# Performance work log

Measured on AMD Instinct MI355X. Metric: run time of the kernel, lower is better.

## Reference

```python
import jax, jax.numpy as jnp
import numpy as np

B, NQ, NK, D = 8, 2048, 2048, 1024

def setup_inputs() -> dict:
    key = jax.random.key(0)
    k1, k2, k3, k4, k5 = jax.random.split(key, 5)
    query_input = jax.random.normal(k1, (B, NQ, D), dtype=jnp.float32)
    key_input = jax.random.normal(k2, (B, NK, D), dtype=jnp.float32)
    s = 1.0 / np.sqrt(D)
    # nn.Linear(in,out,bias=False): y = x @ W.T, W shape (out,in)
    Wq = jax.random.uniform(k3, (D, D), dtype=jnp.float32, minval=-s, maxval=s)
    Wk = jax.random.uniform(k4, (D, D), dtype=jnp.float32, minval=-s, maxval=s)
    Wv = jax.random.uniform(k5, (D, D), dtype=jnp.float32, minval=-s, maxval=s)
    return {"query_input": query_input, "key_input": key_input,
            "Wq": Wq, "Wk": Wk, "Wv": Wv}

def reference(query_input, key_input, Wq, Wk, Wv):
    d = query_input.shape[-1]
    q = jnp.einsum('bnd,ed->bne', query_input, Wq)   # (b, n_q, d)
    k = jnp.einsum('bmd,ed->bme', key_input, Wk)     # (b, n_k, d)
    v = jnp.einsum('bnd,ed->bne', query_input, Wv)   # (b, n_q, d) -- value from query_input
    # scores: K @ Q^T -> (b, n_k, n_q), softmax over n_q
    a = jnp.einsum('bmd,bnd->bmn', k, q) / jnp.sqrt(jnp.float32(d))
    a = jax.nn.softmax(a, axis=-1)
    context = jnp.einsum('bmn,bnd->bmd', a, v)       # (b, n_k, d)
    return context + key_input
```

## Files before the change

### kernel.cpp

```cpp
#include <hip/hip_runtime.h>
#include <hip/hip_bf16.h>

using bf16 = __bf16;
typedef __bf16 bf16x8 __attribute__((ext_vector_type(8)));
typedef float f32x4 __attribute__((ext_vector_type(4)));

__device__ __forceinline__ void gload_lds16(const bf16* g, bf16* l) {
  __builtin_amdgcn_global_load_lds(
      (const __attribute__((address_space(1))) void*)g,
      (__attribute__((address_space(3))) void*)l, 16, 0, 0);
}

__device__ __forceinline__ void cvt8(const float* __restrict__ in,
                                     bf16* __restrict__ out, long i) {
  float4 f0 = *(const float4*)&in[i];
  float4 f1 = *(const float4*)&in[i + 4];
  bf16x8 o;
  o[0] = (bf16)f0.x; o[1] = (bf16)f0.y; o[2] = (bf16)f0.z; o[3] = (bf16)f0.w;
  o[4] = (bf16)f1.x; o[5] = (bf16)f1.y; o[6] = (bf16)f1.z; o[7] = (bf16)f1.w;
  *(bf16x8*)&out[i] = o;
}

__global__ __launch_bounds__(256) void cvt_f32_bf16(const float* __restrict__ in,
                                                    bf16* __restrict__ out, int n) {
  int i = (blockIdx.x * 256 + threadIdx.x) * 8;
  if (i < n) cvt8(in, out, i);
}

__global__ __launch_bounds__(256)
void prep(const float* __restrict__ q, bf16* __restrict__ qb,
          const float* __restrict__ k, bf16* __restrict__ kb,
          const float* __restrict__ wv, bf16* __restrict__ wvb,
          const float* __restrict__ Wq, bf16* __restrict__ WqTb,
          const float* __restrict__ Wk, bf16* __restrict__ WkTb,
          float* __restrict__ GTf, float* __restrict__ rs) {
  __shared__ float tile[64][65];
  const int b = blockIdx.x;
  const int t = threadIdx.x;
  if (b < 8192) { cvt8(q, qb, ((long)b * 256 + t) * 8); return; }
  if (b < 16384) { cvt8(k, kb, ((long)(b - 8192) * 256 + t) * 8); return; }
  if (b < 16896) { cvt8(wv, wvb, ((long)(b - 16384) * 256 + t) * 8); return; }
  if (b < 17408) {
    const int idx = b - 16896;
    const float* in = (idx & 1) ? Wk : Wq;
    bf16* out = (idx & 1) ? WkTb : WqTb;
    const int r0 = ((idx >> 1) & 15) * 64, c0 = (idx >> 5) * 64;
    const int r = t >> 4, c4 = (t & 15) * 4;
#pragma unroll
    for (int rr = 0; rr < 64; rr += 16) {
      float4 v = *(const float4*)&in[(long)(r0 + r + rr) * 1024 + c0 + c4];
      tile[r + rr][c4 + 0] = v.x; tile[r + rr][c4 + 1] = v.y;
      tile[r + rr][c4 + 2] = v.z; tile[r + rr][c4 + 3] = v.w;
    }
    __syncthreads();
    const int cc = t >> 2, rseg = (t & 3) * 16;
    bf16 tmp[16];
#pragma unroll
    for (int kk = 0; kk < 16; ++kk) tmp[kk] = (bf16)tile[rseg + kk][cc];
    *(bf16x8*)&out[(long)(c0 + cc) * 1024 + r0 + rseg] = *(bf16x8*)&tmp[0];
    *(bf16x8*)&out[(long)(c0 + cc) * 1024 + r0 + rseg + 8] = *(bf16x8*)&tmp[8];
    return;
  }
  const int zb = b - 17408;
  if (zb < 1024) *(float4*)&GTf[((long)zb * 256 + t) * 4] = make_float4(0, 0, 0, 0);
  else           *(float4*)&rs[((long)(zb - 1024) * 256 + t) * 4] = make_float4(0, 0, 0, 0);
}

__global__ __launch_bounds__(256)
void gemm_small_atomic(const bf16* __restrict__ A, const bf16* __restrict__ B,
                       float* __restrict__ C, int lda, int ldb, int ldc) {
  const int tid = threadIdx.x;
  const int wave = tid >> 6;
  const int lane = tid & 63;
  const int wr = wave >> 1, wc = wave & 1;
  const long brow = (long)blockIdx.x * 128;
  const long bcol = (long)blockIdx.y * 128;
  const int kofs = blockIdx.z * 256;

  __shared__ bf16 As[128 * 32];
  __shared__ bf16 Bs[128 * 32];
  f32x4 acc[4][4] = {};

  const int r0 = tid >> 2;
  const int c0 = (tid & 3) * 8;
  const bf16* ga = A + (brow + r0) * (long)lda + kofs + c0;
  const bf16* gb = B + (bcol + r0) * (long)ldb + kofs + c0;
  bf16* la0 = As + tid * 8;
  bf16* la1 = As + 2048 + tid * 8;
  bf16* lb0 = Bs + tid * 8;
  bf16* lb1 = Bs + 2048 + tid * 8;
  const int afo = (wr * 64 + (lane & 15)) * 32 + (lane >> 4) * 8;
  const int bfo = (wc * 64 + (lane & 15)) * 32 + (lane >> 4) * 8;

  for (int kt = 0; kt < 8; ++kt) {
    gload_lds16(ga, la0);
    gload_lds16(ga + (long)64 * lda, la1);
    gload_lds16(gb, lb0);
    gload_lds16(gb + (long)64 * ldb, lb1);
    ga += 32; gb += 32;
    __syncthreads();
    bf16x8 av[4], bv[4];
#pragma unroll
    for (int i = 0; i < 4; ++i) {
      av[i] = *(const bf16x8*)&As[afo + i * 512];
      bv[i] = *(const bf16x8*)&Bs[bfo + i * 512];
    }
#pragma unroll
    for (int mi = 0; mi < 4; ++mi)
#pragma unroll
      for (int ni = 0; ni < 4; ++ni)
        acc[mi][ni] = __builtin_amdgcn_mfma_f32_16x16x32_bf16(av[mi], bv[ni],
                                                              acc[mi][ni], 0, 0, 0);
    __syncthreads();
  }

  const int or0 = wr * 64 + ((lane >> 4) << 2);
  const int oc0 = wc * 64 + (lane & 15);
#pragma unroll
  for (int mi = 0; mi < 4; ++mi)
#pragma unroll
    for (int ni = 0; ni < 4; ++ni)
#pragma unroll
      for (int j = 0; j < 4; ++j)
        atomicAdd(&C[(brow + or0 + mi * 16 + j) * ldc + bcol + oc0 + ni * 16],
                  acc[mi][ni][j]);
}

__device__ __forceinline__ void load_frags(const bf16* __restrict__ buf,
                                           int wr, int wc, int lk, int lr,
                                           bf16x8 (&R)[12]) {
#pragma unroll
  for (int mi = 0; mi < 8; ++mi) {
    const int r = wr * 128 + mi * 16 + lr;
    R[mi] = *(const bf16x8*)&buf[r * 32 + ((lk ^ ((r >> 1) & 3)) << 3)];
  }
#pragma unroll
  for (int ni = 0; ni < 4; ++ni) {
    const int r = wc * 64 + ni * 16 + lr;
    R[8 + ni] = *(const bf16x8*)&buf[8192 + r * 32 + ((lk ^ ((r >> 1) & 3)) << 3)];
  }
}

__device__ __forceinline__ void mfma_tile(const bf16x8 (&R)[12], f32x4 (&acc)[8][4]) {
  __builtin_amdgcn_s_setprio(1);
#pragma unroll
  for (int mi = 0; mi < 8; ++mi)
#pragma unroll
    for (int ni = 0; ni < 4; ++ni)
      acc[mi][ni] = __builtin_amdgcn_mfma_f32_16x16x32_bf16(R[mi], R[8 + ni], acc[mi][ni], 0, 0, 0);
  __builtin_amdgcn_s_setprio(0);
}

__device__ __forceinline__ void gemm_mainloop(const bf16* __restrict__ A,
                                              const bf16* __restrict__ B,
                                              int K, int lda, int ldb,
                                              long brow, long bcol,
                                              bf16 (*lds)[16384],
                                              f32x4 (&acc)[8][4]) {
  const int tid = threadIdx.x;
  const int lane = tid & 63;
  const int wave = tid >> 6;
  const int wr = wave >> 2, wc = wave & 3;
  const int srow = tid >> 2;
  const int scg  = (tid & 3) ^ ((srow >> 1) & 3);
  const bf16* gA = A + (brow + srow) * (long)lda + scg * 8;
  const bf16* gB = B + (bcol + srow) * (long)ldb + scg * 8;
  const long a128 = (long)lda << 7;
  const long b128 = (long)ldb << 7;
  const int nk = K >> 5;

  auto stage = [&](int t) {
    bf16* buf = (bf16*)lds[t & 3];
    const bf16* a = gA + (long)t * 32;
    const bf16* b = gB + (long)t * 32;
    gload_lds16(a,        buf + tid * 8);
    gload_lds16(a + a128, buf + 4096 + tid * 8);
    gload_lds16(b,        buf + 8192 + tid * 8);
    gload_lds16(b + b128, buf + 12288 + tid * 8);
  };

  const int lk = lane >> 4;
  const int lr = lane & 15;

  stage(0); stage(1); stage(2);
  asm volatile("s_waitcnt vmcnt(4)" ::: "memory");
  __builtin_amdgcn_s_barrier();

  bf16x8 R0[12], R1[12];
  load_frags((const bf16*)lds[0], wr, wc, lk, lr, R0);

  for (int t = 0; t < nk; t += 2) {
    load_frags((const bf16*)lds[(t + 1) & 3], wr, wc, lk, lr, R1);
    if (t + 3 < nk) stage(t + 3);
    mfma_tile(R0, acc);
    if (t + 3 < nk) { asm volatile("s_waitcnt vmcnt(4)" ::: "memory"); }
    else            { asm volatile("s_waitcnt vmcnt(0)" ::: "memory"); }
    __builtin_amdgcn_s_barrier();
    if (t + 2 < nk) load_frags((const bf16*)lds[(t + 2) & 3], wr, wc, lk, lr, R0);
    if (t + 4 < nk) stage(t + 4);
    mfma_tile(R1, acc);
    if (t + 4 < nk) { asm volatile("s_waitcnt vmcnt(4)" ::: "memory"); }
    else            { asm volatile("s_waitcnt vmcnt(0)" ::: "memory"); }
    __builtin_amdgcn_s_barrier();
  }
}

template <int EPI>
__global__ __launch_bounds__(512, 2)
void gemm_bt(const bf16* __restrict__ A, const bf16* __restrict__ B,
             void* __restrict__ Cv, const bf16* __restrict__ Add,
             float* __restrict__ RS,
             int K, int lda, int ldb, int ldc,
             long sA, long sB, long sC, long sAdd, float scale) {
  int bx = blockIdx.x, by = blockIdx.y, bz = blockIdx.z;
  {
    const int gx = gridDim.x, gxy = gx * gridDim.y;
    const int nwg = gxy * gridDim.z;
    int lin = bx + gx * by + gxy * bz;
    lin = (lin & 7) * (nwg >> 3) + (lin >> 3);
    bz = lin / gxy; const int rem = lin - bz * gxy;
    by = rem / gx;  bx = rem - by * gx;
  }
  __shared__ bf16 lds[4][16384];
  f32x4 acc[8][4] = {};
  gemm_mainloop(A + (long)bz * sA, B + (long)bz * sB, K, lda, ldb,
                (long)bx * 256, (long)by * 256, lds, acc);

  const int lane = threadIdx.x & 63;
  const int wave = threadIdx.x >> 6;
  const int wr = wave >> 2, wc = wave & 3;
  const long brow = (long)bx * 256, bcol = (long)by * 256;
  const int or0 = wr * 128 + ((lane >> 4) << 2);
  const int oc0 = wc * 64 + (lane & 15);
#pragma unroll
  for (int mi = 0; mi < 8; ++mi) {
#pragma unroll
    for (int j = 0; j < 4; ++j) {
      const long row = brow + or0 + mi * 16 + j;
      if constexpr (EPI == 1) {
        bf16* C = (bf16*)Cv + (long)bz * sC;
        float s = 0.f;
#pragma unroll
        for (int ni = 0; ni < 4; ++ni) {
          const float e = __expf(acc[mi][ni][j] * scale);
          s += e;
          C[row * ldc + bcol + oc0 + ni * 16] = (bf16)e;
        }
        s += __shfl_xor(s, 1, 64); s += __shfl_xor(s, 2, 64);
        s += __shfl_xor(s, 4, 64); s += __shfl_xor(s, 8, 64);
        if ((lane & 15) == 0) atomicAdd(&RS[(long)bz * 2048 + row], s);
      } else {
        float* C = (float*)Cv + (long)bz * sC;
        const bf16* Ad = Add + (long)bz * sAdd;
        const float iv = 1.0f / RS[(long)bz * 2048 + row];
#pragma unroll
        for (int ni = 0; ni < 4; ++ni) {
          const long col = bcol + oc0 + ni * 16;
          C[row * ldc + col] = acc[mi][ni][j] * iv + (float)Ad[row * ldc + col];
        }
      }
    }
  }
}

__global__ __launch_bounds__(512, 2)
void gemm_fused_t1vpt(const bf16* __restrict__ kb, const bf16* __restrict__ GTb,
                      bf16* __restrict__ T1, const bf16* __restrict__ Wvb,
                      const bf16* __restrict__ qb, bf16* __restrict__ Vpt) {
  int id = blockIdx.x;
  id = (id & 7) * 64 + (id >> 3);
  const bf16 *A, *B; bf16* C; int ldc; long brow, bcol;
  if (id < 256) {
    A = kb; B = GTb; C = T1; ldc = 1024;
    brow = (long)(id & 63) * 256; bcol = (long)(id >> 6) * 256;
  } else {
    const int j = id - 256;
    const int bz = j >> 5;
    A = Wvb; B = qb + (long)bz * 2097152; C = Vpt + (long)bz * 2097152; ldc = 2048;
    brow = (long)(j & 3) * 256; bcol = (long)((j >> 2) & 7) * 256;
  }
  __shared__ bf16 lds[4][16384];
  f32x4 acc[8][4] = {};
  gemm_mainloop(A, B, 1024, 1024, 1024, brow, bcol, lds, acc);

  const int lane = threadIdx.x & 63;
  const int wave = threadIdx.x >> 6;
  const int wr = wave >> 2, wc = wave & 3;
  const int or0 = wr * 128 + ((lane >> 4) << 2);
  const int oc0 = wc * 64 + (lane & 15);
#pragma unroll
  for (int mi = 0; mi < 8; ++mi)
#pragma unroll
    for (int j = 0; j < 4; ++j) {
      const long row = brow + or0 + mi * 16 + j;
#pragma unroll
      for (int ni = 0; ni < 4; ++ni)
        C[row * ldc + bcol + oc0 + ni * 16] = (bf16)acc[mi][ni][j];
    }
}

extern "C" void kernel_launch(void* const* d_in, const int* in_sizes, int n_in,
                              void* d_out, int out_size, void* d_ws, size_t ws_size,
                              hipStream_t stream) {
  const float* q_in = (const float*)d_in[0];
  const float* k_in = (const float*)d_in[1];
  const float* Wq   = (const float*)d_in[2];
  const float* Wk   = (const float*)d_in[3];
  const float* Wv   = (const float*)d_in[4];
  float* out = (float*)d_out;
  char* ws = (char*)d_ws;

  bf16*  qb   = (bf16*)(ws);
  bf16*  kb   = (bf16*)(ws + 33554432);
  bf16*  S    = (bf16*)(ws + 67108864);
  float* GTf  = (float*)(ws + 67108864);
  bf16*  GTb  = (bf16*)(ws + 71303168);
  bf16*  T1   = (bf16*)(ws + 134217728);
  bf16*  Wvb  = (bf16*)(ws + 167772160);
  bf16*  WqTb = (bf16*)(ws + 169869312);
  bf16*  WkTb = (bf16*)(ws + 171966464);
  float* rs   = (float*)(ws + 174063616);
  bf16*  Vpt  = (bf16*)(ws + 176160768);

  prep<<<18448, 256, 0, stream>>>(q_in, qb, k_in, kb, Wv, Wvb,
                                  Wq, WqTb, Wk, WkTb, GTf, rs);

  gemm_small_atomic<<<dim3(8, 8, 4), 256, 0, stream>>>(WqTb, WkTb, GTf, 1024, 1024, 1024);
  cvt_f32_bf16<<<512, 256, 0, stream>>>(GTf, GTb, 1048576);

  gemm_fused_t1vpt<<<512, 512, 0, stream>>>(kb, GTb, T1, Wvb, qb, Vpt);

  gemm_bt<1><<<dim3(8, 8, 8), 512, 0, stream>>>(
      T1, qb, S, nullptr, rs, 1024, 1024, 1024, 2048,
      2097152L, 2097152L, 4194304L, 0L, 0.03125f);

  gemm_bt<2><<<dim3(8, 4, 8), 512, 0, stream>>>(
      S, Vpt, out, kb, rs, 2048, 2048, 2048, 1024,
      4194304L, 2097152L, 2097152L, 2097152L, 1.0f);
}
```

Before: 283.6 us.

## Quantize attention probabilities and values to FP8 and run PV GEMM with FP8 MFMA

The score kernel now writes exp(scores) as software-converted e4m3 bytes and accumulates the row sum from the dequantized values. The value projection is also stored as e4m3. A new FP8 GEMM kernel uses the 16x16x32 fp8 MFMA with byte-sized LDS tiles, which halves operand traffic for the largest GEMM and uses higher-throughput matrix instructions. Separately, the small Wq^T·Wk GEMM is split into more K-slices with more atomic adds. This trades accuracy for speed: e4m3 on unnormalized exp values and on V may exceed the tolerance, and values below 2^-6 are flushed to zero.

```diff
diff --git a/kernel.cpp b/kernel.cpp
--- a/kernel.cpp
+++ b/kernel.cpp
@@ -5,10 +5,27 @@
 typedef __bf16 bf16x8 __attribute__((ext_vector_type(8)));
 typedef float f32x4 __attribute__((ext_vector_type(4)));
 
-__device__ __forceinline__ void gload_lds16(const bf16* g, bf16* l) {
+__device__ __forceinline__ void gload16(const void* g, void* l) {
   __builtin_amdgcn_global_load_lds(
       (const __attribute__((address_space(1))) void*)g,
       (__attribute__((address_space(3))) void*)l, 16, 0, 0);
+}
+
+__device__ __forceinline__ unsigned char f32_e4m3(float f) {
+  unsigned u = __float_as_uint(f);
+  unsigned s = (u >> 24) & 0x80u;
+  unsigned a = u & 0x7fffffffu;
+  if (a < 0x3c800000u) return (unsigned char)s;
+  if (a > 0x43e00000u) return (unsigned char)(s | 0x7eu);
+  unsigned r = a + 0x0007ffffu + ((a >> 20) & 1u);
+  unsigned e = (r >> 23) - 120u;
+  unsigned m = (r >> 20) & 7u;
+  return (unsigned char)(s | (e << 3) | m);
+}
+__device__ __forceinline__ float e4m3_f32(unsigned char b) {
+  if (!(b & 0x78u)) return 0.f;
+  return __uint_as_float(((((unsigned)(b >> 3) & 15u) + 120u) << 23) |
+                         (((unsigned)b & 7u) << 20));
 }
 
 __device__ __forceinline__ void cvt8(const float* __restrict__ in,
@@ -75,7 +92,7 @@
   const int wr = wave >> 1, wc = wave & 1;
   const long brow = (long)blockIdx.x * 128;
   const long bcol = (long)blockIdx.y * 128;
-  const int kofs = blockIdx.z * 256;
+  const int kofs = blockIdx.z * 128;
 
   __shared__ bf16 As[128 * 32];
   __shared__ bf16 Bs[128 * 32];
@@ -92,11 +109,11 @@
   const int afo = (wr * 64 + (lane & 15)) * 32 + (lane >> 4) * 8;
   const int bfo = (wc * 64 + (lane & 15)) * 32 + (lane >> 4) * 8;
 
-  for (int kt = 0; kt < 8; ++kt) {
-    gload_lds16(ga, la0);
-    gload_lds16(ga + (long)64 * lda, la1);
-    gload_lds16(gb, lb0);
-    gload_lds16(gb + (long)64 * ldb, lb1);
+  for (int kt = 0; kt < 4; ++kt) {
+    gload16(ga, la0);
+    gload16(ga + (long)64 * lda, la1);
+    gload16(gb, lb0);
+    gload16(gb + (long)64 * ldb, lb1);
     ga += 32; gb += 32;
     __syncthreads();
     bf16x8 av[4], bv[4];
@@ -173,10 +190,10 @@
     bf16* buf = (bf16*)lds[t & 3];
     const bf16* a = gA + (long)t * 32;
     const bf16* b = gB + (long)t * 32;
-    gload_lds16(a,        buf + tid * 8);
-    gload_lds16(a + a128, buf + 4096 + tid * 8);
-    gload_lds16(b,        buf + 8192 + tid * 8);
-    gload_lds16(b + b128, buf + 12288 + tid * 8);
+    gload16(a,        buf + tid * 8);
+    gload16(a + a128, buf + 4096 + tid * 8);
+    gload16(b,        buf + 8192 + tid * 8);
+    gload16(b + b128, buf + 12288 + tid * 8);
   };
 
   const int lk = lane >> 4;
@@ -205,13 +222,10 @@
   }
 }
 
-template <int EPI>
 __global__ __launch_bounds__(512, 2)
-void gemm_bt(const bf16* __restrict__ A, const bf16* __restrict__ B,
-             void* __restrict__ Cv, const bf16* __restrict__ Add,
-             float* __restrict__ RS,
-             int K, int lda, int ldb, int ldc,
-             long sA, long sB, long sC, long sAdd, float scale) {
+void gemm_scores(const bf16* __restrict__ T1, const bf16* __restrict__ qb,
+                 unsigned char* __restrict__ S8, float* __restrict__ RS,
+                 float scale) {
   int bx = blockIdx.x, by = blockIdx.y, bz = blockIdx.z;
   {
     const int gx = gridDim.x, gxy = gx * gridDim.y;
@@ -223,8 +237,8 @@
   }
   __shared__ bf16 lds[4][16384];
   f32x4 acc[8][4] = {};
-  gemm_mainloop(A + (long)bz * sA, B + (long)bz * sB, K, lda, ldb,
-                (long)bx * 256, (long)by * 256, lds, acc);
+  gemm_mainloop(T1 + (long)bz * 2097152, qb + (long)bz * 2097152,
+                1024, 1024, 1024, (long)bx * 256, (long)by * 256, lds, acc);
 
   const int lane = threadIdx.x & 63;
   const int wave = threadIdx.x >> 6;
@@ -232,33 +246,22 @@
   const long brow = (long)bx * 256, bcol = (long)by * 256;
   const int or0 = wr * 128 + ((lane >> 4) << 2);
   const int oc0 = wc * 64 + (lane & 15);
+  unsigned char* S = S8 + (long)bz * 4194304;
 #pragma unroll
   for (int mi = 0; mi < 8; ++mi) {
 #pragma unroll
     for (int j = 0; j < 4; ++j) {
       const long row = brow + or0 + mi * 16 + j;
-      if constexpr (EPI == 1) {
-        bf16* C = (bf16*)Cv + (long)bz * sC;
-        float s = 0.f;
-#pragma unroll
-        for (int ni = 0; ni < 4; ++ni) {
-          const float e = __expf(acc[mi][ni][j] * scale);
-          s += e;
-          C[row * ldc + bcol + oc0 + ni * 16] = (bf16)e;
-        }
-        s += __shfl_xor(s, 1, 64); s += __shfl_xor(s, 2, 64);
-        s += __shfl_xor(s, 4, 64); s += __shfl_xor(s, 8, 64);
-        if ((lane & 15) == 0) atomicAdd(&RS[(long)bz * 2048 + row], s);
-      } else {
-        float* C = (float*)Cv + (long)bz * sC;
-        const bf16* Ad = Add + (long)bz * sAdd;
-        const float iv = 1.0f / RS[(long)bz * 2048 + row];
-#pragma unroll
-        for (int ni = 0; ni < 4; ++ni) {
-          const long col = bcol + oc0 + ni * 16;
-          C[row * ldc + col] = acc[mi][ni][j] * iv + (float)Ad[row * ldc + col];
-        }
+      float s = 0.f;
+#pragma unroll
+      for (int ni = 0; ni < 4; ++ni) {
+        const unsigned char q = f32_e4m3(__expf(acc[mi][ni][j] * scale));
+        S[row * 2048 + bcol + oc0 + ni * 16] = q;
+        s += e4m3_f32(q);
       }
+      s += __shfl_xor(s, 1, 64); s += __shfl_xor(s, 2, 64);
+      s += __shfl_xor(s, 4, 64); s += __shfl_xor(s, 8, 64);
+      if ((lane & 15) == 0) atomicAdd(&RS[(long)bz * 2048 + row], s);
     }
   }
 }
@@ -266,17 +269,17 @@
 __global__ __launch_bounds__(512, 2)
 void gemm_fused_t1vpt(const bf16* __restrict__ kb, const bf16* __restrict__ GTb,
                       bf16* __restrict__ T1, const bf16* __restrict__ Wvb,
-                      const bf16* __restrict__ qb, bf16* __restrict__ Vpt) {
+                      const bf16* __restrict__ qb, unsigned char* __restrict__ V8) {
   int id = blockIdx.x;
   id = (id & 7) * 64 + (id >> 3);
-  const bf16 *A, *B; bf16* C; int ldc; long brow, bcol;
-  if (id < 256) {
-    A = kb; B = GTb; C = T1; ldc = 1024;
+  const bf16 *A, *B; long brow, bcol; int isT1 = (id < 256); int bz = 0;
+  if (isT1) {
+    A = kb; B = GTb;
     brow = (long)(id & 63) * 256; bcol = (long)(id >> 6) * 256;
   } else {
     const int j = id - 256;
-    const int bz = j >> 5;
-    A = Wvb; B = qb + (long)bz * 2097152; C = Vpt + (long)bz * 2097152; ldc = 2048;
+    bz = j >> 5;
+    A = Wvb; B = qb + (long)bz * 2097152;
     brow = (long)(j & 3) * 256; bcol = (long)((j >> 2) & 7) * 256;
   }
   __shared__ bf16 lds[4][16384];
@@ -294,9 +297,110 @@
     for (int j = 0; j < 4; ++j) {
       const long row = brow + or0 + mi * 16 + j;
 #pragma unroll
+      for (int ni = 0; ni < 4; ++ni) {
+        const long col = bcol + oc0 + ni * 16;
+        if (isT1) T1[row * 1024 + col] = (bf16)acc[mi][ni][j];
+        else      V8[(long)bz * 2097152 + row * 2048 + col] = f32_e4m3(acc[mi][ni][j]);
+      }
+    }
+}
+
+__global__ __launch_bounds__(512, 2)
+void gemm_pv8(const unsigned char* __restrict__ S8, const unsigned char* __restrict__ V8,
+              float* __restrict__ out, const bf16* __restrict__ kb,
+              const float* __restrict__ RS) {
+  int bx = blockIdx.x, by = blockIdx.y, bz = blockIdx.z;
+  {
+    const int gx = gridDim.x, gxy = gx * gridDim.y;
+    const int nwg = gxy * gridDim.z;
+    int lin = bx + gx * by + gxy * bz;
+    lin = (lin & 7) * (nwg >> 3) + (lin >> 3);
+    bz = lin / gxy; const int rem = lin - bz * gxy;
+    by = rem / gx;  bx = rem - by * gx;
+  }
+  const unsigned char* A = S8 + (long)bz * 4194304;
+  const unsigned char* B = V8 + (long)bz * 2097152;
+  const int tid = threadIdx.x;
+  const int lane = tid & 63;
+  const int wave = tid >> 6;
+  const int wr = wave >> 2, wc = wave & 3;
+  const long brow = (long)bx * 256, bcol = (long)by * 256;
+
+  __shared__ unsigned char lds8[4][16384];
+  f32x4 acc[8][4] = {};
+
+  const int srow = tid >> 1;
+  const int sc   = (tid & 1) * 16;
+  const unsigned char* gA = A + (brow + srow) * 2048 + sc;
+  const unsigned char* gB = B + (bcol + srow) * 2048 + sc;
+
+  auto stage = [&](int t) {
+    unsigned char* buf = lds8[t & 3];
+    gload16(gA + (long)t * 32, buf + tid * 16);
+    gload16(gB + (long)t * 32, buf + 8192 + tid * 16);
+  };
+
+  const int lk = lane >> 4;
+  const int lr = lane & 15;
+
+  auto loadf = [&](const unsigned char* buf, long (&R)[12]) {
+#pragma unroll
+    for (int mi = 0; mi < 8; ++mi)
+      R[mi] = *(const long*)&buf[(wr * 128 + mi * 16 + lr) * 32 + lk * 8];
+#pragma unroll
+    for (int ni = 0; ni < 4; ++ni)
+      R[8 + ni] = *(const long*)&buf[8192 + (wc * 64 + ni * 16 + lr) * 32 + lk * 8];
+  };
+  auto mf = [&](const long (&R)[12]) {
+    __builtin_amdgcn_s_setprio(1);
+#pragma unroll
+    for (int mi = 0; mi < 8; ++mi)
+#pragma unroll
       for (int ni = 0; ni < 4; ++ni)
-        C[row * ldc + bcol + oc0 + ni * 16] = (bf16)acc[mi][ni][j];
+        acc[mi][ni] = __builtin_amdgcn_mfma_f32_16x16x32_fp8_fp8(R[mi], R[8 + ni], acc[mi][ni], 0, 0, 0);
+    __builtin_amdgcn_s_setprio(0);
+  };
+
+  const int nk = 64;
+  stage(0); stage(1); stage(2);
+  asm volatile("s_waitcnt vmcnt(2)" ::: "memory");
+  __builtin_amdgcn_s_barrier();
+
+  long R0[12], R1[12];
+  loadf(lds8[0], R0);
+
+  for (int t = 0; t < nk; t += 2) {
+    loadf(lds8[(t + 1) & 3], R1);
+    if (t + 3 < nk) stage(t + 3);
+    mf(R0);
+    if (t + 3 < nk) { asm volatile("s_waitcnt vmcnt(2)" ::: "memory"); }
+    else            { asm volatile("s_waitcnt vmcnt(0)" ::: "memory"); }
+    __builtin_amdgcn_s_barrier();
+    if (t + 2 < nk) loadf(lds8[(t + 2) & 3], R0);
+    if (t + 4 < nk) stage(t + 4);
+    mf(R1);
+    if (t + 4 < nk) { asm volatile("s_waitcnt vmcnt(2)" ::: "memory"); }
+    else            { asm volatile("s_waitcnt vmcnt(0)" ::: "memory"); }
+    __builtin_amdgcn_s_barrier();
+  }
+
+  const int or0 = wr * 128 + ((lane >> 4) << 2);
+  const int oc0 = wc * 64 + (lane & 15);
+  float* C = out + (long)bz * 2097152;
+  const bf16* Ad = kb + (long)bz * 2097152;
+#pragma unroll
+  for (int mi = 0; mi < 8; ++mi) {
+#pragma unroll
+    for (int j = 0; j < 4; ++j) {
+      const long row = brow + or0 + mi * 16 + j;
+      const float iv = 1.0f / RS[(long)bz * 2048 + row];
+#pragma unroll
+      for (int ni = 0; ni < 4; ++ni) {
+        const long col = bcol + oc0 + ni * 16;
+        C[row * 1024 + col] = acc[mi][ni][j] * iv + (float)Ad[row * 1024 + col];
+      }
     }
+  }
 }
 
 extern "C" void kernel_launch(void* const* d_in, const int* in_sizes, int n_in,
@@ -312,29 +416,25 @@
 
   bf16*  qb   = (bf16*)(ws);
   bf16*  kb   = (bf16*)(ws + 33554432);
-  bf16*  S    = (bf16*)(ws + 67108864);
-  float* GTf  = (float*)(ws + 67108864);
-  bf16*  GTb  = (bf16*)(ws + 71303168);
+  unsigned char* S8 = (unsigned char*)(ws + 67108864);
+  float* GTf  = (float*)(ws + 100663296);
+  bf16*  GTb  = (bf16*)(ws + 104857600);
   bf16*  T1   = (bf16*)(ws + 134217728);
   bf16*  Wvb  = (bf16*)(ws + 167772160);
   bf16*  WqTb = (bf16*)(ws + 169869312);
   bf16*  WkTb = (bf16*)(ws + 171966464);
   float* rs   = (float*)(ws + 174063616);
-  bf16*  Vpt  = (bf16*)(ws + 176160768);
+  unsigned char* V8 = (unsigned char*)(ws + 176160768);
 
   prep<<<18448, 256, 0, stream>>>(q_in, qb, k_in, kb, Wv, Wvb,
                                   Wq, WqTb, Wk, WkTb, GTf, rs);
 
-  gemm_small_atomic<<<dim3(8, 8, 4), 256, 0, stream>>>(WqTb, WkTb, GTf, 1024, 1024, 1024);
+  gemm_small_atomic<<<dim3(8, 8, 8), 256, 0, stream>>>(WqTb, WkTb, GTf, 1024, 1024, 1024);
   cvt_f32_bf16<<<512, 256, 0, stream>>>(GTf, GTb, 1048576);
 
-  gemm_fused_t1vpt<<<512, 512, 0, stream>>>(kb, GTb, T1, Wvb, qb, Vpt);
-
-  gemm_bt<1><<<dim3(8, 8, 8), 512, 0, stream>>>(
-      T1, qb, S, nullptr, rs, 1024, 1024, 1024, 2048,
-      2097152L, 2097152L, 4194304L, 0L, 0.03125f);
-
-  gemm_bt<2><<<dim3(8, 4, 8), 512, 0, stream>>>(
-      S, Vpt, out, kb, rs, 2048, 2048, 2048, 1024,
-      4194304L, 2097152L, 2097152L, 2097152L, 1.0f);
-}
+  gemm_fused_t1vpt<<<512, 512, 0, stream>>>(kb, GTb, T1, Wvb, qb, V8);
+
+  gemm_scores<<<dim3(8, 8, 8), 512, 0, stream>>>(T1, qb, S8, rs, 0.03125f);
+
+  gemm_pv8<<<dim3(8, 4, 8), 512, 0, stream>>>(S8, V8, out, kb, rs);
+}
```

After: 319.3 us. 1.13x slower.
